# Kernel tuning notes

Hardware: AMD Instinct MI355X
Metric: run time of the kernel (lower is better)

The kernel has to match this reference:

```python
import jax, jax.numpy as jnp
import numpy as np

A, N, D, H, ADIM = 8, 32768, 128, 4, 32  # agents, batch, hidden, heads, attend_dim


def setup_inputs() -> dict:
    key = jax.random.key(0)
    ks = jax.random.split(key, 7)
    querys = jax.random.normal(ks[0], (A, N, D), jnp.float32)
    keys = jax.random.normal(ks[1], (A, N, D), jnp.float32)
    values = jax.random.normal(ks[2], (A, N, D), jnp.float32)
    s = 1.0 / np.sqrt(D)
    Wk = jax.random.normal(ks[3], (H, ADIM, D), jnp.float32) * s   # key_extractors (no bias)
    Wsel = jax.random.normal(ks[4], (H, ADIM, D), jnp.float32) * s  # selector_extractors (no bias)
    Wv = jax.random.normal(ks[5], (H, ADIM, D), jnp.float32) * s   # value_extractors Linear
    bv = jax.random.normal(ks[6], (H, ADIM), jnp.float32) * s      # value_extractors bias
    return {"querys": querys, "keys": keys, "values": values,
            "Wk": Wk, "Wsel": Wsel, "Wv": Wv, "bv": bv}


def _offdiag_idx(a):
    # idx[i, j] enumerates the a-1 agents != i, in order (matches torch list comp j != a_i)
    j = jnp.arange(a - 1)[None, :]
    i = jnp.arange(a)[:, None]
    return jnp.where(j < i, j, j + 1)  # [A, A-1]


def reference(querys, keys, values, Wk, Wsel, Wv, bv):
    # per-head projections: [H, A, N, K]
    hk = jnp.einsum('and,hkd->hank', keys, Wk)
    hs = jnp.einsum('and,hkd->hank', querys, Wsel)
    hv = jax.nn.leaky_relu(jnp.einsum('and,hkd->hank', values, Wv) + bv[:, None, None, :],
                           negative_slope=0.01)
    # full logits over all key-agents j for each query-agent i: [H, A, N, A]
    logits_full = jnp.einsum('hink,hjnk->hinj', hs, hk)
    scale = 1.0 / jnp.sqrt(jnp.asarray(hk.shape[-1], hk.dtype))
    # self-exclusion: mask j == i so softmax over j equals softmax over the other agents
    self_mask = jnp.eye(A, dtype=bool)[None, :, None, :]
    probs_full = jax.nn.softmax(jnp.where(self_mask, -1e9, logits_full * scale), axis=-1)
    # attended values: [H, A, N, K] (diagonal prob is exactly 0 after masking? it is ~e^{-1e9} ~ 0)
    other = jnp.einsum('hinj,hjnk->hink', probs_full, hv)
    # gather the self-excluded logits/probs in the original (A-1)-length layout
    idx = _offdiag_idx(A)
    idx4 = jnp.broadcast_to(idx[None, :, None, :], logits_full.shape[:-1] + (A - 1,))
    logits_ex = jnp.take_along_axis(logits_full, idx4, axis=-1)  # [H, A, N, A-1]
    probs_ex = jnp.take_along_axis(probs_full, idx4, axis=-1)    # [H, A, N, A-1]
    # reorder to agent-major like the torch nested lists: [A, H, ...]
    return (jnp.swapaxes(other, 0, 1),
            jnp.swapaxes(logits_ex, 0, 1),
            jnp.swapaxes(probs_ex, 0, 1))
```

## Files before the change

kernel.cpp:

```cpp
#include <hip/hip_runtime.h>
#include <hip/hip_bf16.h>

typedef unsigned short u16;
typedef unsigned int u32;

#define AGT 8
#define NBATCH 32768
#define DDIM 128
#define HEADS 4
#define KDIM 32
#define CC 128
#define NT 8
#define MROWS 64

typedef float f32x4 __attribute__((ext_vector_type(4)));
typedef float f32x2 __attribute__((ext_vector_type(2)));
typedef __bf16 bf16x8 __attribute__((ext_vector_type(8)));
typedef short s16x8 __attribute__((ext_vector_type(8)));
typedef u32 u32x4 __attribute__((ext_vector_type(4)));

union FragU { s16x8 s; bf16x8 b; u32x4 u; };

__device__ __forceinline__ u16 f2bf(float f) {
  u32 u = __float_as_uint(f);
  u = (u + 0x7FFFu + ((u >> 16) & 1u)) >> 16;
  return (u16)u;
}

__device__ __forceinline__ u32 cvtpk(float lo, float hi) {
  u32 r;
  asm("v_cvt_pk_bf16_f32 %0, %1, %2" : "=v"(r) : "v"(lo), "v"(hi));
  return r;
}

__device__ __forceinline__ f32x2 bfpair(u32 u) {
  f32x2 r;
  r.x = __uint_as_float(u << 16);
  r.y = __uint_as_float(u & 0xFFFF0000u);
  return r;
}

__global__ void prep_weights(const float* __restrict__ Wk,
                             const float* __restrict__ Ws,
                             const float* __restrict__ Wv,
                             u16* __restrict__ Wb) {
  int idx = blockIdx.x * 256 + threadIdx.x;
  if (idx >= 3 * 8 * 4 * 64 * 8) return;
  int b  = idx & 7;
  int l  = (idx >> 3) & 63;
  int kc = (idx >> 9) & 3;
  int ct = (idx >> 11) & 7;
  int pj = idx >> 14;
  int c = ct * 16 + (l & 15);
  int h = c >> 5, kk = c & 31;
  int d = kc * 32 + ((b >> 2) << 4) + ((l >> 4) << 2) + (b & 3);
  const float* W = (pj == 0) ? Wk : ((pj == 1) ? Ws : Wv);
  Wb[idx] = f2bf(W[(h * KDIM + kk) * DDIM + d]);
}

__global__ __launch_bounds__(256, 3) void fused_attn(
    const float* __restrict__ qin, const float* __restrict__ kin,
    const float* __restrict__ vin, const u16* __restrict__ Wb,
    const float* __restrict__ bv,
    float* __restrict__ out0, float* __restrict__ out1,
    float* __restrict__ out2) {
  __shared__ __align__(16) u16 sH[3][MROWS * CC];

  const int tid = threadIdx.x;
  const int l = tid & 63;
  const int w = tid >> 6;
  const int n0 = blockIdx.x * NT;
  const int lr = l & 15;
  const int lg = l >> 4;

  const int arow = w * 16 + lr;
  const size_t grow_off =
      ((size_t)(arow >> 3) * NBATCH + (size_t)(n0 + (arow & 7))) * DDIM;

  FragU fa[3][4];
#pragma unroll
  for (int pj = 0; pj < 3; ++pj) {
    const float* X = (pj == 0) ? kin : ((pj == 1) ? qin : vin);
    const float* grow = X + grow_off;
#pragma unroll
    for (int kc = 0; kc < 4; ++kc) {
      const float4 x0 = *(const float4*)(grow + kc * 32 + lg * 4);
      const float4 x1 = *(const float4*)(grow + kc * 32 + lg * 4 + 16);
      u32x4 t;
      t[0] = cvtpk(x0.x, x0.y);
      t[1] = cvtpk(x0.z, x0.w);
      t[2] = cvtpk(x1.x, x1.y);
      t[3] = cvtpk(x1.z, x1.w);
      fa[pj][kc].u = t;
    }
  }

#pragma unroll
  for (int pj = 0; pj < 3; ++pj) {
    f32x4 acc[8];
#pragma unroll
    for (int ct = 0; ct < 8; ++ct) acc[ct] = (f32x4)(0.0f);

#pragma unroll
    for (int ct = 0; ct < 8; ++ct) {
#pragma unroll
      for (int kc = 0; kc < 4; ++kc) {
        FragU fb;
        fb.s = *(const s16x8*)(Wb + ((((pj * 8 + ct) * 4 + kc) * 64 + l) << 3));
        acc[ct] = __builtin_amdgcn_mfma_f32_16x16x32_bf16(fa[pj][kc].b, fb.b,
                                                          acc[ct], 0, 0, 0);
      }
    }

    u16* dst = sH[pj];
#pragma unroll
    for (int ct = 0; ct < 8; ++ct) {
      const int c = ct * 16 + lr;
      float x[4];
#pragma unroll
      for (int rg = 0; rg < 4; ++rg) x[rg] = acc[ct][rg];
      if (pj == 2) {
        const float bias = bv[c];
#pragma unroll
        for (int rg = 0; rg < 4; ++rg) {
          float v = x[rg] + bias;
          x[rg] = (v > 0.0f) ? v : 0.01f * v;
        }
      }
      const u32 p01 = cvtpk(x[0], x[1]);
      const u32 p23 = cvtpk(x[2], x[3]);
      const int rb = w * 16 + lg * 4;
      const int cb = c * 2;
#pragma unroll
      for (int rg = 0; rg < 4; ++rg) {
        const int row = rb + rg;
        const u32 pk = (rg < 2) ? p01 : p23;
        const u16 val = (rg & 1) ? (u16)(pk >> 16) : (u16)pk;
        *(u16*)((char*)dst + row * 256 + (cb ^ ((row & 7) << 4))) = val;
      }
    }
  }

  __syncthreads();

  const int h = w;
  const int i = l >> 3;
  const int nt = l & 7;
  const int n = n0 + nt;
  const int cb2 = h * 64;

  f32x2 hs2[16];
  {
    const int r = i * 8 + nt;
    const int swz = (r & 7) << 4;
#pragma unroll
    for (int qc = 0; qc < 4; ++qc) {
      u32x4 ch = *(const u32x4*)((const char*)sH[1] + r * 256 +
                                 ((cb2 + qc * 16) ^ swz));
#pragma unroll
      for (int e = 0; e < 4; ++e) hs2[qc * 4 + e] = bfpair(ch[e]);
    }
  }

  float logits[8];
#pragma unroll
  for (int j = 0; j < 8; ++j) {
    const int r = j * 8 + nt;
    const int swz = (r & 7) << 4;
    f32x2 a2 = (f32x2)(0.0f);
#pragma unroll
    for (int qc = 0; qc < 4; ++qc) {
      u32x4 ch = *(const u32x4*)((const char*)sH[0] + r * 256 +
                                 ((cb2 + qc * 16) ^ swz));
#pragma unroll
      for (int e = 0; e < 4; ++e) a2 = bfpair(ch[e]) * hs2[qc * 4 + e] + a2;
    }
    logits[j] = a2.x + a2.y;
  }

  const float scale = 0.17677669529663687f;
  float sl[8];
#pragma unroll
  for (int j = 0; j < 8; ++j) sl[j] = (j == i) ? -1e30f : logits[j] * scale;
  float m = sl[0];
#pragma unroll
  for (int j = 1; j < 8; ++j) m = fmaxf(m, sl[j]);
  float p[8];
  float s = 0.0f;
#pragma unroll
  for (int j = 0; j < 8; ++j) { p[j] = __expf(sl[j] - m); s += p[j]; }
  const float inv = 1.0f / s;

  const size_t ob = ((size_t)(i * HEADS + h) * NBATCH + (size_t)n);
  const size_t ob7 = ob * 7;
#pragma unroll
  for (int j = 0; j < 8; ++j) {
    if (j != i) {
      const int jj = j - ((j > i) ? 1 : 0);
      out1[ob7 + jj] = logits[j];
      out2[ob7 + jj] = p[j] * inv;
    }
  }

  f32x2 o2[16];
#pragma unroll
  for (int e = 0; e < 16; ++e) o2[e] = (f32x2)(0.0f);
#pragma unroll
  for (int j = 0; j < 8; ++j) {
    const float pw = p[j] * inv;
    const f32x2 pw2 = (f32x2)(pw);
    const int r = j * 8 + nt;
    const int swz = (r & 7) << 4;
#pragma unroll
    for (int qc = 0; qc < 4; ++qc) {
      u32x4 ch = *(const u32x4*)((const char*)sH[2] + r * 256 +
                                 ((cb2 + qc * 16) ^ swz));
#pragma unroll
      for (int e = 0; e < 4; ++e)
        o2[qc * 4 + e] = bfpair(ch[e]) * pw2 + o2[qc * 4 + e];
    }
  }

  const size_t o0 = ob * 32;
#pragma unroll
  for (int g = 0; g < 8; ++g) {
    float4 vv = make_float4(o2[g * 2].x, o2[g * 2].y,
                            o2[g * 2 + 1].x, o2[g * 2 + 1].y);
    *(float4*)(out0 + o0 + g * 4) = vv;
  }
}

extern "C" void kernel_launch(void* const* d_in, const int* in_sizes, int n_in,
                              void* d_out, int out_size, void* d_ws,
                              size_t ws_size, hipStream_t stream) {
  const float* qin = (const float*)d_in[0];
  const float* kin = (const float*)d_in[1];
  const float* vin = (const float*)d_in[2];
  const float* Wk  = (const float*)d_in[3];
  const float* Ws  = (const float*)d_in[4];
  const float* Wv  = (const float*)d_in[5];
  const float* bvp = (const float*)d_in[6];

  float* out0 = (float*)d_out;
  float* out1 = out0 + (size_t)AGT * HEADS * NBATCH * KDIM;
  float* out2 = out1 + (size_t)AGT * HEADS * NBATCH * 7;

  u16* Wb = (u16*)d_ws;

  prep_weights<<<dim3(192), dim3(256), 0, stream>>>(Wk, Ws, Wv, Wb);
  fused_attn<<<dim3(NBATCH / NT), dim3(256), 0, stream>>>(
      qin, kin, vin, Wb, bvp, out0, out1, out2);
}
```

Before: 274.3 us.

## Halve batch tile per block and split head dimension across lane pairs

Each block now covers 4 batch items instead of 8. Waves split the projection output columns two ways, and pairs of lanes each handle half of the 32-wide head dimension, combining their partial logits with a shuffle. This cuts shared memory and register use per block so occupancy can go from 3 to 6 blocks per CU, and spreads the output stores of logits and probs across both lanes of a pair. In exchange there are twice as many blocks, so the weight fragments are reloaded more often per batch item, and a cross-lane shuffle is added.

Result: no change. 273.2 us (-0.4%).

```diff
diff --git a/kernel.cpp b/kernel.cpp
--- a/kernel.cpp
+++ b/kernel.cpp
@@ -10,8 +10,8 @@
 #define HEADS 4
 #define KDIM 32
 #define CC 128
-#define NT 8
-#define MROWS 64
+#define NT 4
+#define MROWS 32
 
 typedef float f32x4 __attribute__((ext_vector_type(4)));
 typedef float f32x2 __attribute__((ext_vector_type(2)));
@@ -58,7 +58,7 @@
   Wb[idx] = f2bf(W[(h * KDIM + kk) * DDIM + d]);
 }
 
-__global__ __launch_bounds__(256, 3) void fused_attn(
+__global__ __launch_bounds__(256, 6) void fused_attn(
     const float* __restrict__ qin, const float* __restrict__ kin,
     const float* __restrict__ vin, const u16* __restrict__ Wb,
     const float* __restrict__ bv,
@@ -72,16 +72,19 @@
   const int n0 = blockIdx.x * NT;
   const int lr = l & 15;
   const int lg = l >> 4;
-
-  const int arow = w * 16 + lr;
+  const int wr = w >> 1;
+  const int wc = w & 1;
+
+  const int arow = wr * 16 + lr;
   const size_t grow_off =
-      ((size_t)(arow >> 3) * NBATCH + (size_t)(n0 + (arow & 7))) * DDIM;
-
-  FragU fa[3][4];
+      ((size_t)(arow >> 2) * NBATCH + (size_t)(n0 + (arow & 3))) * DDIM;
+
 #pragma unroll
   for (int pj = 0; pj < 3; ++pj) {
     const float* X = (pj == 0) ? kin : ((pj == 1) ? qin : vin);
     const float* grow = X + grow_off;
+
+    FragU fa[4];
 #pragma unroll
     for (int kc = 0; kc < 4; ++kc) {
       const float4 x0 = *(const float4*)(grow + kc * 32 + lg * 4);
@@ -91,31 +94,29 @@
       t[1] = cvtpk(x0.z, x0.w);
       t[2] = cvtpk(x1.x, x1.y);
       t[3] = cvtpk(x1.z, x1.w);
-      fa[pj][kc].u = t;
-    }
-  }
-
-#pragma unroll
-  for (int pj = 0; pj < 3; ++pj) {
-    f32x4 acc[8];
-#pragma unroll
-    for (int ct = 0; ct < 8; ++ct) acc[ct] = (f32x4)(0.0f);
-
-#pragma unroll
-    for (int ct = 0; ct < 8; ++ct) {
+      fa[kc].u = t;
+    }
+
+    f32x4 acc[4];
+#pragma unroll
+    for (int ct = 0; ct < 4; ++ct) acc[ct] = (f32x4)(0.0f);
+
+#pragma unroll
+    for (int ct = 0; ct < 4; ++ct) {
+      const int ctg = wc * 4 + ct;
 #pragma unroll
       for (int kc = 0; kc < 4; ++kc) {
         FragU fb;
-        fb.s = *(const s16x8*)(Wb + ((((pj * 8 + ct) * 4 + kc) * 64 + l) << 3));
-        acc[ct] = __builtin_amdgcn_mfma_f32_16x16x32_bf16(fa[pj][kc].b, fb.b,
+        fb.s = *(const s16x8*)(Wb + ((((pj * 8 + ctg) * 4 + kc) * 64 + l) << 3));
+        acc[ct] = __builtin_amdgcn_mfma_f32_16x16x32_bf16(fa[kc].b, fb.b,
                                                           acc[ct], 0, 0, 0);
       }
     }
 
     u16* dst = sH[pj];
 #pragma unroll
-    for (int ct = 0; ct < 8; ++ct) {
-      const int c = ct * 16 + lr;
+    for (int ct = 0; ct < 4; ++ct) {
+      const int c = (wc * 4 + ct) * 16 + lr;
       float x[4];
 #pragma unroll
       for (int rg = 0; rg < 4; ++rg) x[rg] = acc[ct][rg];
@@ -129,7 +130,7 @@
       }
       const u32 p01 = cvtpk(x[0], x[1]);
       const u32 p23 = cvtpk(x[2], x[3]);
-      const int rb = w * 16 + lg * 4;
+      const int rb = wr * 16 + lg * 4;
       const int cb = c * 2;
 #pragma unroll
       for (int rg = 0; rg < 4; ++rg) {
@@ -145,18 +146,19 @@
 
   const int h = w;
   const int i = l >> 3;
-  const int nt = l & 7;
+  const int nt = (l >> 1) & 3;
+  const int half = l & 1;
   const int n = n0 + nt;
-  const int cb2 = h * 64;
-
-  f32x2 hs2[16];
+  const int cb = h * 64 + half * 32;
+
+  f32x2 hs2[8];
   {
-    const int r = i * 8 + nt;
+    const int r = i * 4 + nt;
     const int swz = (r & 7) << 4;
 #pragma unroll
-    for (int qc = 0; qc < 4; ++qc) {
+    for (int qc = 0; qc < 2; ++qc) {
       u32x4 ch = *(const u32x4*)((const char*)sH[1] + r * 256 +
-                                 ((cb2 + qc * 16) ^ swz));
+                                 ((cb + qc * 16) ^ swz));
 #pragma unroll
       for (int e = 0; e < 4; ++e) hs2[qc * 4 + e] = bfpair(ch[e]);
     }
@@ -165,17 +167,18 @@
   float logits[8];
 #pragma unroll
   for (int j = 0; j < 8; ++j) {
-    const int r = j * 8 + nt;
+    const int r = j * 4 + nt;
     const int swz = (r & 7) << 4;
     f32x2 a2 = (f32x2)(0.0f);
 #pragma unroll
-    for (int qc = 0; qc < 4; ++qc) {
+    for (int qc = 0; qc < 2; ++qc) {
       u32x4 ch = *(const u32x4*)((const char*)sH[0] + r * 256 +
-                                 ((cb2 + qc * 16) ^ swz));
+                                 ((cb + qc * 16) ^ swz));
 #pragma unroll
       for (int e = 0; e < 4; ++e) a2 = bfpair(ch[e]) * hs2[qc * 4 + e] + a2;
     }
-    logits[j] = a2.x + a2.y;
+    const float part = a2.x + a2.y;
+    logits[j] = part + __shfl_xor(part, 1);
   }
 
   const float scale = 0.17677669529663687f;
@@ -193,37 +196,46 @@
 
   const size_t ob = ((size_t)(i * HEADS + h) * NBATCH + (size_t)n);
   const size_t ob7 = ob * 7;
-#pragma unroll
-  for (int j = 0; j < 8; ++j) {
-    if (j != i) {
-      const int jj = j - ((j > i) ? 1 : 0);
-      out1[ob7 + jj] = logits[j];
-      out2[ob7 + jj] = p[j] * inv;
-    }
-  }
-
-  f32x2 o2[16];
-#pragma unroll
-  for (int e = 0; e < 16; ++e) o2[e] = (f32x2)(0.0f);
+  if (half == 0) {
+#pragma unroll
+    for (int j = 0; j < 8; ++j) {
+      if (j != i) {
+        const int jj = j - ((j > i) ? 1 : 0);
+        out1[ob7 + jj] = logits[j];
+      }
+    }
+  } else {
+#pragma unroll
+    for (int j = 0; j < 8; ++j) {
+      if (j != i) {
+        const int jj = j - ((j > i) ? 1 : 0);
+        out2[ob7 + jj] = p[j] * inv;
+      }
+    }
+  }
+
+  f32x2 o2[8];
+#pragma unroll
+  for (int e = 0; e < 8; ++e) o2[e] = (f32x2)(0.0f);
 #pragma unroll
   for (int j = 0; j < 8; ++j) {
     const float pw = p[j] * inv;
     const f32x2 pw2 = (f32x2)(pw);
-    const int r = j * 8 + nt;
+    const int r = j * 4 + nt;
     const int swz = (r & 7) << 4;
 #pragma unroll
-    for (int qc = 0; qc < 4; ++qc) {
+    for (int qc = 0; qc < 2; ++qc) {
       u32x4 ch = *(const u32x4*)((const char*)sH[2] + r * 256 +
-                                 ((cb2 + qc * 16) ^ swz));
+                                 ((cb + qc * 16) ^ swz));
 #pragma unroll
       for (int e = 0; e < 4; ++e)
         o2[qc * 4 + e] = bfpair(ch[e]) * pw2 + o2[qc * 4 + e];
     }
   }
 
-  const size_t o0 = ob * 32;
-#pragma unroll
-  for (int g = 0; g < 8; ++g) {
+  const size_t o0 = ob * 32 + half * 16;
+#pragma unroll
+  for (int g = 0; g < 4; ++g) {
     float4 vv = make_float4(o2[g * 2].x, o2[g * 2].y,
                             o2[g * 2 + 1].x, o2[g * 2 + 1].y);
     *(float4*)(out0 + o0 + g * 4) = vv;
```
